# Optimization experiments

Hardware: AMD Instinct MI355X
Metric: run time of the kernel (lower is better)

## Reference

```python
import jax, jax.numpy as jnp
import numpy as np

NFREQ = 5


def setup_inputs() -> dict:
    key = jax.random.key(0)
    k1, k2 = jax.random.split(key)
    B, H, T, F = 16, 16, 1024, 64
    x = jax.random.normal(k1, (B, H, T, F), dtype=jnp.float32)
    # Conv3D kernel: (1, k0, k1, in_ch=F, out_ch=F) as in keras DHWIO layout
    W = jax.random.normal(k2, (1, 3, 3, F, F), dtype=jnp.float32) * 0.05
    b = jnp.zeros((F,), dtype=jnp.float32)
    return {"x": x, "W": W, "b": b}


def _conv3d_relu(x5, W, b):
    # x5: [B, H, P, Q, F]; W: [1, k0, k1, F, F]; 'same' padding, stride 1
    y = jax.lax.conv_general_dilated(
        x5, W, window_strides=(1, 1, 1), padding='SAME',
        dimension_numbers=('NDHWC', 'DHWIO', 'NDHWC'))
    return jax.nn.relu(y + b)


def reference(x, W, b):
    B, H, T, F = x.shape
    freq_list = np.arange(1, T // 2, T // 2 // NFREQ)  # static python ints
    # amplitude: |rfft over T|, mean over F -> [B, H, T//2+1]
    amp = jnp.mean(jnp.abs(jnp.fft.rfft(x, axis=2)), axis=-1)
    period_weight = amp[:, :, freq_list]              # [B, H, nfreq]
    pw = jax.nn.softmax(period_weight, axis=-1)       # [B, H, nfreq]

    res = []
    for p in (freq_list + 1):
        p = int(p)
        q = int(np.ceil(T / p))                       # segments per period
        pad = q * p - T
        xt = jnp.pad(x, ((0, 0), (0, 0), (0, pad), (0, 0)))
        x5 = xt.reshape(B, H, p, q, F)                # [B,H,p,q,F]
        y = _conv3d_relu(x5, W, b)                    # [B,H,p,q,F]
        y = y.reshape(B, H, p * q, F)[:, :, :T, :]    # crop back to T
        res.append(y)
    res = jnp.stack(res, axis=-1)                     # [B,H,T,F,nfreq]
    out = jnp.sum(res * pw[:, :, None, None, :], axis=-1) + x
    return out
```

## Files before the change

### kernel.cpp

```cpp
#include <hip/hip_runtime.h>

typedef __attribute__((ext_vector_type(8))) short bhalf8;
typedef __attribute__((ext_vector_type(4))) float floatx4;

#define NF 6

__device__ __forceinline__ unsigned short f2bf(float f) {
  unsigned u = __float_as_uint(f);
  u += 0x7FFFu + ((u >> 16) & 1u);
  return (unsigned short)(u >> 16);
}

__global__ __launch_bounds__(512) void pw_kernel(const float* __restrict__ x,
                                                 float* __restrict__ pwbuf) {
  const int bh = blockIdx.x;
  const int tid = threadIdx.x;
  const int w = tid >> 6;
  const int f = tid & 63;
  const int t0w = w * 128;
  const float* xb = x + (size_t)bh * 65536 + f;

  const float STEP = -6.283185307179586f / 1024.0f;
  float re[NF], im[NF], c[NF], s[NF], ck[NF], sk[NF];
#pragma unroll
  for (int k = 0; k < NF; ++k) {
    int freq = 1 + 102 * k;
    int ph0 = (freq * t0w) & 1023;
    __sincosf((float)ph0 * STEP, &s[k], &c[k]);
    __sincosf((float)freq * STEP, &sk[k], &ck[k]);
    re[k] = 0.f;
    im[k] = 0.f;
  }
#pragma unroll 4
  for (int t = 0; t < 128; ++t) {
    float v = xb[(size_t)(t0w + t) * 64];
#pragma unroll
    for (int k = 0; k < NF; ++k) {
      re[k] = fmaf(v, c[k], re[k]);
      im[k] = fmaf(v, s[k], im[k]);
      float cn = fmaf(c[k], ck[k], -s[k] * sk[k]);
      float sn = fmaf(c[k], sk[k], s[k] * ck[k]);
      c[k] = cn;
      s[k] = sn;
    }
  }
  __shared__ float part[8][NF][64][2];
#pragma unroll
  for (int k = 0; k < NF; ++k) {
    part[w][k][f][0] = re[k];
    part[w][k][f][1] = im[k];
  }
  __syncthreads();
  if (tid < 64) {
    float sm[NF];
#pragma unroll
    for (int k = 0; k < NF; ++k) {
      float rr = 0.f, ii = 0.f;
#pragma unroll
      for (int ww = 0; ww < 8; ++ww) {
        rr += part[ww][k][tid][0];
        ii += part[ww][k][tid][1];
      }
      float amp = sqrtf(rr * rr + ii * ii);
#pragma unroll
      for (int off = 32; off > 0; off >>= 1) amp += __shfl_xor(amp, off);
      sm[k] = amp * (1.0f / 64.0f);
    }
    if (tid == 0) {
      float m = sm[0];
#pragma unroll
      for (int i = 1; i < NF; ++i) m = fmaxf(m, sm[i]);
      float e[NF], ssum = 0.f;
#pragma unroll
      for (int i = 0; i < NF; ++i) {
        e[i] = __expf(sm[i] - m);
        ssum += e[i];
      }
      float inv = 1.0f / ssum;
#pragma unroll
      for (int i = 0; i < NF; ++i) pwbuf[bh * NF + i] = e[i] * inv;
    }
  }
}

__global__ void prep_w(const float* __restrict__ W,
                       unsigned short* __restrict__ wt_img) {
  int task = blockIdx.x * 256 + threadIdx.x;
  int didj = task >> 9;
  int fo = (task >> 3) & 63;
  int c = task & 7;
  int cs = c ^ (fo & 7);
  bhalf8 pk;
#pragma unroll
  for (int j = 0; j < 8; ++j) {
    int fi = cs * 8 + j;
    pk[j] = (short)f2bf(W[(size_t)(didj * 64 + fi) * 64 + fo]);
  }
  *(bhalf8*)((char*)wt_img + (size_t)didj * 8192 + fo * 128 + c * 16) = pk;
}

__global__ __launch_bounds__(512, 2) void conv_kernel(
    const float* __restrict__ x, const unsigned short* __restrict__ wt_img,
    const float* __restrict__ bias, const float* __restrict__ pwbuf,
    float* __restrict__ out) {
  __shared__ __align__(16) unsigned short win[152 * 64];
  __shared__ __align__(16) unsigned short farw[132 * 64];
  __shared__ __align__(16) unsigned short wl[9 * 64 * 64];

  const int tid = threadIdx.x;
  const int bh = blockIdx.y;
  const int t0 = blockIdx.x * 128;
  const float* xbh = x + (size_t)bh * (1024 * 64);

  {
    const int fi0 = (tid & 7) * 8;
#pragma unroll
    for (int rr = 0; rr < 3; ++rr) {
      int trel = (tid >> 3) + rr * 64;
      if (trel < 152) {
        int tp = t0 - 12 + trel;
        float va[8];
        if ((unsigned)tp < 1024u) {
          const float4* src = (const float4*)(xbh + (size_t)tp * 64 + fi0);
          float4 u0 = src[0], u1 = src[1];
          va[0] = u0.x; va[1] = u0.y; va[2] = u0.z; va[3] = u0.w;
          va[4] = u1.x; va[5] = u1.y; va[6] = u1.z; va[7] = u1.w;
        } else {
#pragma unroll
          for (int j = 0; j < 8; ++j) va[j] = 0.f;
        }
        bhalf8 pk;
#pragma unroll
        for (int j = 0; j < 8; ++j) pk[j] = (short)f2bf(va[j]);
        *(bhalf8*)((char*)win + (trel << 7) +
                   ((fi0 * 2) ^ ((trel & 7) << 4))) = pk;
      }
    }
    const int fb = (t0 < 512) ? (t0 + 510) : (t0 - 514);
#pragma unroll
    for (int rr = 0; rr < 3; ++rr) {
      int trel = (tid >> 3) + rr * 64;
      if (trel < 132) {
        int tp = fb + trel;
        float va[8];
        if ((unsigned)tp < 1024u) {
          const float4* src = (const float4*)(xbh + (size_t)tp * 64 + fi0);
          float4 u0 = src[0], u1 = src[1];
          va[0] = u0.x; va[1] = u0.y; va[2] = u0.z; va[3] = u0.w;
          va[4] = u1.x; va[5] = u1.y; va[6] = u1.z; va[7] = u1.w;
        } else {
#pragma unroll
          for (int j = 0; j < 8; ++j) va[j] = 0.f;
        }
        bhalf8 pk;
#pragma unroll
        for (int j = 0; j < 8; ++j) pk[j] = (short)f2bf(va[j]);
        *(bhalf8*)((char*)farw + (trel << 7) +
                   ((fi0 * 2) ^ ((trel & 7) << 4))) = pk;
      }
    }
#pragma unroll
    for (int d = 0; d < 9; ++d) {
      const char* src = (const char*)wt_img + (size_t)d * 8192;
      char* dst = (char*)wl + (size_t)d * 8192;
      *(bhalf8*)(dst + tid * 16) = *(const bhalf8*)(src + tid * 16);
    }
  }
  __syncthreads();

  const int l15 = tid & 15;
  const int l4 = (tid >> 4) & 3;
  const int wid = tid >> 6;
  const int wm = (wid >> 1) * 32;
  const int wc = wid & 1;
  const int vdi = (t0 < 512) ? 2 : 0;

  const int rt0 = t0 + wm + l15, rt1 = rt0 + 16;
  int jma[NF], jmb[NF];
  jma[0] = rt0 & 511;  jmb[0] = rt1 & 511;
  jma[1] = rt0 % 10;   jmb[1] = rt1 % 10;
  jma[2] = rt0 % 5;    jmb[2] = rt1 % 5;
  jma[3] = rt0 % 4;    jmb[3] = rt1 % 4;
  jma[4] = rt0 % 3;    jmb[4] = rt1 % 3;
  jma[5] = rt0 & 1;    jmb[5] = rt1 & 1;

  floatx4 acc[NF][2][2];
#pragma unroll
  for (int kp = 0; kp < NF; ++kp)
#pragma unroll
    for (int mt = 0; mt < 2; ++mt)
#pragma unroll
      for (int nt = 0; nt < 2; ++nt) acc[kp][mt][nt] = (floatx4)0.0f;

  const bhalf8 zz = (bhalf8)0;

#define DO_TAP(KP, BUF, R0, Q)                                                \
  {                                                                           \
    bool ok0 = (dj == 0) ? (jma[KP] > 0)                                      \
               : (dj == 2) ? (jma[KP] < (Q) - 1) : true;                      \
    bool ok1 = (dj == 0) ? (jmb[KP] > 0)                                      \
               : (dj == 2) ? (jmb[KP] < (Q) - 1) : true;                      \
    int r0_ = (R0), r1_ = r0_ + 16;                                           \
    _Pragma("unroll") for (int kk = 0; kk < 2; ++kk) {                        \
      int kb = kk * 64 + l4 * 16;                                             \
      bhalf8 a0 = *(const bhalf8*)((const char*)(BUF) + (r0_ << 7) +          \
                                   (kb ^ ((r0_ & 7) << 4)));                  \
      bhalf8 a1 = *(const bhalf8*)((const char*)(BUF) + (r1_ << 7) +          \
                                   (kb ^ ((r1_ & 7) << 4)));                  \
      if (!ok0) a0 = zz;                                                      \
      if (!ok1) a1 = zz;                                                      \
      _Pragma("unroll") for (int nt = 0; nt < 2; ++nt) {                      \
        acc[KP][0][nt] = __builtin_amdgcn_mfma_f32_16x16x32_bf16(             \
            a0, bfr[kk][nt], acc[KP][0][nt], 0, 0, 0);                        \
        acc[KP][1][nt] = __builtin_amdgcn_mfma_f32_16x16x32_bf16(             \
            a1, bfr[kk][nt], acc[KP][1][nt], 0, 0, 0);                        \
      }                                                                       \
    }                                                                         \
  }

#pragma unroll
  for (int di = 0; di < 3; ++di) {
#pragma unroll
    for (int dj = 0; dj < 3; ++dj) {
      bhalf8 bfr[2][2];
      const char* wt = (const char*)wl + (size_t)(di * 3 + dj) * 8192;
#pragma unroll
      for (int kk = 0; kk < 2; ++kk)
#pragma unroll
        for (int nt = 0; nt < 2; ++nt) {
          int fo = wc * 32 + nt * 16 + l15;
          bfr[kk][nt] = *(const bhalf8*)(wt + (fo << 7) +
                                         ((kk * 64 + l4 * 16) ^
                                          ((fo & 7) << 4)));
        }
      const int base = wm + l15;
      if (di == 1) {
        DO_TAP(0, win, base + 11 + dj, 512)
      } else if (di == vdi) {
        DO_TAP(0, farw, base + dj + 1, 512)
      }
      DO_TAP(1, win, base + 12 + (di - 1) * 10 + dj - 1, 10)
      DO_TAP(2, win, base + 12 + (di - 1) * 5 + dj - 1, 5)
      DO_TAP(3, win, base + 12 + (di - 1) * 4 + dj - 1, 4)
      DO_TAP(4, win, base + 12 + (di - 1) * 3 + dj - 1, 3)
      DO_TAP(5, win, base + 12 + (di - 1) * 2 + dj - 1, 2)
    }
  }
#undef DO_TAP

  float pwv[NF];
#pragma unroll
  for (int kp = 0; kp < NF; ++kp) pwv[kp] = pwbuf[bh * NF + kp];
  float bv[2];
#pragma unroll
  for (int nt = 0; nt < 2; ++nt) bv[nt] = bias[wc * 32 + nt * 16 + l15];

#pragma unroll
  for (int mt = 0; mt < 2; ++mt) {
#pragma unroll
    for (int nt = 0; nt < 2; ++nt) {
      int row = t0 + wm + mt * 16 + l4 * 4;
      int col = wc * 32 + nt * 16 + l15;
      size_t basep = ((size_t)bh * 1024 + row) * 64 + col;
#pragma unroll
      for (int r = 0; r < 4; ++r) {
        float y = 0.f;
#pragma unroll
        for (int kp = 0; kp < NF; ++kp)
          y = fmaf(pwv[kp], fmaxf(acc[kp][mt][nt][r] + bv[nt], 0.f), y);
        out[basep + (size_t)r * 64] = y + x[basep + (size_t)r * 64];
      }
    }
  }
}

extern "C" void kernel_launch(void* const* d_in, const int* in_sizes, int n_in,
                              void* d_out, int out_size, void* d_ws,
                              size_t ws_size, hipStream_t stream) {
  const float* x = (const float*)d_in[0];
  const float* W = (const float*)d_in[1];
  const float* b = (const float*)d_in[2];
  float* out = (float*)d_out;
  float* pwbuf = (float*)d_ws;
  unsigned short* wt_img = (unsigned short*)((char*)d_ws + 8192);

  pw_kernel<<<dim3(256), dim3(512), 0, stream>>>(x, pwbuf);
  prep_w<<<dim3(18), dim3(256), 0, stream>>>(W, wt_img);
  conv_kernel<<<dim3(8, 256), dim3(512), 0, stream>>>(x, wt_img, b, pwbuf, out);
}
```

Before: 140.7 us.

## Read conv weights from global memory and raise occupancy to four blocks per CU

The 72KB shared-memory copy of the bf16 weight image is removed, so each tap now reads its B fragments straight from global memory (L1/L2-cached), with the swizzle dropped from the weight layout. This cuts LDS use so the launch bound can ask for four blocks per CU instead of two. Boundary masking becomes precomputed edge bitmasks that redirect out-of-range A loads to a shared zero row instead of selecting zeros after the load. The tap loops are no longer unrolled, which lowers register pressure, but each tap now pays global-load latency and loses some instruction-level parallelism.

New measurement: 370.8 us. +163.5%, slower.

```diff
diff --git a/kernel.cpp b/kernel.cpp
--- a/kernel.cpp
+++ b/kernel.cpp
@@ -89,23 +89,22 @@
   int didj = task >> 9;
   int fo = (task >> 3) & 63;
   int c = task & 7;
-  int cs = c ^ (fo & 7);
   bhalf8 pk;
 #pragma unroll
   for (int j = 0; j < 8; ++j) {
-    int fi = cs * 8 + j;
+    int fi = c * 8 + j;
     pk[j] = (short)f2bf(W[(size_t)(didj * 64 + fi) * 64 + fo]);
   }
   *(bhalf8*)((char*)wt_img + (size_t)didj * 8192 + fo * 128 + c * 16) = pk;
 }
 
-__global__ __launch_bounds__(512, 2) void conv_kernel(
+__global__ __launch_bounds__(512, 4) void conv_kernel(
     const float* __restrict__ x, const unsigned short* __restrict__ wt_img,
     const float* __restrict__ bias, const float* __restrict__ pwbuf,
     float* __restrict__ out) {
   __shared__ __align__(16) unsigned short win[152 * 64];
   __shared__ __align__(16) unsigned short farw[132 * 64];
-  __shared__ __align__(16) unsigned short wl[9 * 64 * 64];
+  __shared__ __align__(16) unsigned short zrow[64];
 
   const int tid = threadIdx.x;
   const int bh = blockIdx.y;
@@ -159,30 +158,41 @@
                    ((fi0 * 2) ^ ((trel & 7) << 4))) = pk;
       }
     }
-#pragma unroll
-    for (int d = 0; d < 9; ++d) {
-      const char* src = (const char*)wt_img + (size_t)d * 8192;
-      char* dst = (char*)wl + (size_t)d * 8192;
-      *(bhalf8*)(dst + tid * 16) = *(const bhalf8*)(src + tid * 16);
-    }
+    if (tid < 8) *(bhalf8*)((char*)zrow + tid * 16) = (bhalf8)0;
   }
   __syncthreads();
 
   const int l15 = tid & 15;
-  const int l4 = (tid >> 4) & 3;
+  const int l4x16 = ((tid >> 4) & 3) * 16;
   const int wid = tid >> 6;
   const int wm = (wid >> 1) * 32;
   const int wc = wid & 1;
   const int vdi = (t0 < 512) ? 2 : 0;
+  const char* zb = (const char*)zrow;
 
   const int rt0 = t0 + wm + l15, rt1 = rt0 + 16;
-  int jma[NF], jmb[NF];
-  jma[0] = rt0 & 511;  jmb[0] = rt1 & 511;
-  jma[1] = rt0 % 10;   jmb[1] = rt1 % 10;
-  jma[2] = rt0 % 5;    jmb[2] = rt1 % 5;
-  jma[3] = rt0 % 4;    jmb[3] = rt1 % 4;
-  jma[4] = rt0 % 3;    jmb[4] = rt1 % 3;
-  jma[5] = rt0 & 1;    jmb[5] = rt1 & 1;
+  int eLo0 = 0, eHi0 = 0, eLo1 = 0, eHi1 = 0;
+  {
+    int j0, j1;
+    j0 = rt0 & 511; j1 = rt1 & 511;
+    eLo0 |= (j0 == 0) << 0;   eHi0 |= (j0 == 511) << 0;
+    eLo1 |= (j1 == 0) << 0;   eHi1 |= (j1 == 511) << 0;
+    j0 = rt0 % 10;  j1 = rt1 % 10;
+    eLo0 |= (j0 == 0) << 1;   eHi0 |= (j0 == 9) << 1;
+    eLo1 |= (j1 == 0) << 1;   eHi1 |= (j1 == 9) << 1;
+    j0 = rt0 % 5;   j1 = rt1 % 5;
+    eLo0 |= (j0 == 0) << 2;   eHi0 |= (j0 == 4) << 2;
+    eLo1 |= (j1 == 0) << 2;   eHi1 |= (j1 == 4) << 2;
+    j0 = rt0 & 3;   j1 = rt1 & 3;
+    eLo0 |= (j0 == 0) << 3;   eHi0 |= (j0 == 3) << 3;
+    eLo1 |= (j1 == 0) << 3;   eHi1 |= (j1 == 3) << 3;
+    j0 = rt0 % 3;   j1 = rt1 % 3;
+    eLo0 |= (j0 == 0) << 4;   eHi0 |= (j0 == 2) << 4;
+    eLo1 |= (j1 == 0) << 4;   eHi1 |= (j1 == 2) << 4;
+    j0 = rt0 & 1;   j1 = rt1 & 1;
+    eLo0 |= (j0 == 0) << 5;   eHi0 |= (j0 == 1) << 5;
+    eLo1 |= (j1 == 0) << 5;   eHi1 |= (j1 == 1) << 5;
+  }
 
   floatx4 acc[NF][2][2];
 #pragma unroll
@@ -192,23 +202,18 @@
 #pragma unroll
       for (int nt = 0; nt < 2; ++nt) acc[kp][mt][nt] = (floatx4)0.0f;
 
-  const bhalf8 zz = (bhalf8)0;
-
-#define DO_TAP(KP, BUF, R0, Q)                                                \
+#define DO_TAP(KP, BUFBASE, R0)                                               \
   {                                                                           \
-    bool ok0 = (dj == 0) ? (jma[KP] > 0)                                      \
-               : (dj == 2) ? (jma[KP] < (Q) - 1) : true;                      \
-    bool ok1 = (dj == 0) ? (jmb[KP] > 0)                                      \
-               : (dj == 2) ? (jmb[KP] < (Q) - 1) : true;                      \
     int r0_ = (R0), r1_ = r0_ + 16;                                           \
+    const char* pa0 =                                                         \
+        (((bad0 >> (KP)) & 1) == 0) ? (const char*)(BUFBASE) + (r0_ << 7) : zb; \
+    const char* pa1 =                                                         \
+        (((bad1 >> (KP)) & 1) == 0) ? (const char*)(BUFBASE) + (r1_ << 7) : zb; \
+    int sw0 = (r0_ & 7) << 4, sw1 = (r1_ & 7) << 4;                           \
     _Pragma("unroll") for (int kk = 0; kk < 2; ++kk) {                        \
-      int kb = kk * 64 + l4 * 16;                                             \
-      bhalf8 a0 = *(const bhalf8*)((const char*)(BUF) + (r0_ << 7) +          \
-                                   (kb ^ ((r0_ & 7) << 4)));                  \
-      bhalf8 a1 = *(const bhalf8*)((const char*)(BUF) + (r1_ << 7) +          \
-                                   (kb ^ ((r1_ & 7) << 4)));                  \
-      if (!ok0) a0 = zz;                                                      \
-      if (!ok1) a1 = zz;                                                      \
+      int kb = kk * 64 + l4x16;                                               \
+      bhalf8 a0 = *(const bhalf8*)(pa0 + (kb ^ sw0));                         \
+      bhalf8 a1 = *(const bhalf8*)(pa1 + (kb ^ sw1));                         \
       _Pragma("unroll") for (int nt = 0; nt < 2; ++nt) {                      \
         acc[KP][0][nt] = __builtin_amdgcn_mfma_f32_16x16x32_bf16(             \
             a0, bfr[kk][nt], acc[KP][0][nt], 0, 0, 0);                        \
@@ -218,32 +223,34 @@
     }                                                                         \
   }
 
-#pragma unroll
+  const int base = wm + l15;
+#pragma unroll 1
   for (int di = 0; di < 3; ++di) {
-#pragma unroll
+#pragma unroll 1
     for (int dj = 0; dj < 3; ++dj) {
       bhalf8 bfr[2][2];
-      const char* wt = (const char*)wl + (size_t)(di * 3 + dj) * 8192;
+      const char* wt = (const char*)wt_img + (size_t)(di * 3 + dj) * 8192;
 #pragma unroll
       for (int kk = 0; kk < 2; ++kk)
 #pragma unroll
         for (int nt = 0; nt < 2; ++nt) {
           int fo = wc * 32 + nt * 16 + l15;
-          bfr[kk][nt] = *(const bhalf8*)(wt + (fo << 7) +
-                                         ((kk * 64 + l4 * 16) ^
-                                          ((fo & 7) << 4)));
+          bfr[kk][nt] =
+              *(const bhalf8*)(wt + (fo << 7) + kk * 64 + l4x16);
         }
-      const int base = wm + l15;
+      int bad0 = (dj == 0) ? eLo0 : (dj == 2) ? eHi0 : 0;
+      int bad1 = (dj == 0) ? eLo1 : (dj == 2) ? eHi1 : 0;
       if (di == 1) {
-        DO_TAP(0, win, base + 11 + dj, 512)
+        DO_TAP(0, win, base + 11 + dj)
       } else if (di == vdi) {
-        DO_TAP(0, farw, base + dj + 1, 512)
-      }
-      DO_TAP(1, win, base + 12 + (di - 1) * 10 + dj - 1, 10)
-      DO_TAP(2, win, base + 12 + (di - 1) * 5 + dj - 1, 5)
-      DO_TAP(3, win, base + 12 + (di - 1) * 4 + dj - 1, 4)
-      DO_TAP(4, win, base + 12 + (di - 1) * 3 + dj - 1, 3)
-      DO_TAP(5, win, base + 12 + (di - 1) * 2 + dj - 1, 2)
+        DO_TAP(0, farw, base + dj + 1)
+      }
+      const int so = di - 1;
+      DO_TAP(1, win, base + 12 + so * 10 + dj - 1)
+      DO_TAP(2, win, base + 12 + so * 5 + dj - 1)
+      DO_TAP(3, win, base + 12 + so * 4 + dj - 1)
+      DO_TAP(4, win, base + 12 + so * 3 + dj - 1)
+      DO_TAP(5, win, base + 12 + so * 2 + dj - 1)
     }
   }
 #undef DO_TAP
@@ -259,7 +266,7 @@
   for (int mt = 0; mt < 2; ++mt) {
 #pragma unroll
     for (int nt = 0; nt < 2; ++nt) {
-      int row = t0 + wm + mt * 16 + l4 * 4;
+      int row = t0 + wm + mt * 16 + ((tid >> 4) & 3) * 4;
       int col = wc * 32 + nt * 16 + l15;
       size_t basep = ((size_t)bh * 1024 + row) * 64 + col;
 #pragma unroll
```
